# Kernel optimization log

Hardware: AMD Instinct MI355X
Metric: run time of the kernel (lower is better)

Reference implementation:

```python
import jax, jax.numpy as jnp
import numpy as np

B, S, H = 4, 8256, 768
NH, HD = 12, 64
W = 128
SHIFT = W // 2  # 64; first SHIFT tokens form their own block after the shift
NW = (S - SHIFT) // W  # 64 full windows
ROPE_BASE = 10000.0


def _rope_cos_sin(length, hd):
    inv_freq = 1.0 / (ROPE_BASE ** (jnp.arange(0, hd, 2, dtype=jnp.float32) / hd))
    ang = jnp.arange(length, dtype=jnp.float32)[:, None] * inv_freq[None, :]  # [L, hd/2]
    return jnp.cos(ang), jnp.sin(ang)


def _apply_rope(x, cos, sin):
    # x: [..., L, hd]; cos/sin: [L, hd/2] (broadcast over leading dims)
    x1, x2 = x[..., : HD // 2], x[..., HD // 2 :]
    return jnp.concatenate([x1 * cos - x2 * sin, x2 * cos + x1 * sin], axis=-1)


def _sdpa(q, k, v):
    # q,k,v: [..., L, hd]; full softmax attention within the block
    scores = jnp.einsum('...qd,...kd->...qk', q, k) / jnp.sqrt(jnp.asarray(HD, q.dtype))
    probs = jax.nn.softmax(scores, axis=-1)
    return jnp.einsum('...qk,...kd->...qd', probs, v)


def setup_inputs() -> dict:
    key = jax.random.key(0)
    ks = jax.random.split(key, 8)
    std = 0.02
    return {
        'hidden_states': jax.random.normal(ks[0], (B, S, H), dtype=jnp.float32),
        'attention_mask': jnp.zeros((B, 1, 1, S), dtype=jnp.float32),
        'Wq': jax.random.normal(ks[1], (H, H), dtype=jnp.float32) * std,
        'bq': jnp.zeros((H,), dtype=jnp.float32),
        'Wk': jax.random.normal(ks[2], (H, H), dtype=jnp.float32) * std,
        'bk': jnp.zeros((H,), dtype=jnp.float32),
        'Wv': jax.random.normal(ks[3], (H, H), dtype=jnp.float32) * std,
        'bv': jnp.zeros((H,), dtype=jnp.float32),
    }


def _global_block(h, Wq, bq, Wk, bk, Wv, bv):
    # h: [B, L, H]; full attention with global-position RoPE (BertSelfAttention.forward)
    L = h.shape[1]
    cos, sin = _rope_cos_sin(L, HD)

    def heads(x):  # [B, L, H] -> [B, NH, L, HD]
        return x.reshape(B, L, NH, HD).transpose(0, 2, 1, 3)

    q = _apply_rope(heads(h @ Wq.T + bq), cos, sin)
    k = _apply_rope(heads(h @ Wk.T + bk), cos, sin)
    v = heads(h @ Wv.T + bv)
    ctx = _sdpa(q, k, v)  # [B, NH, L, HD]
    return ctx.transpose(0, 2, 1, 3).reshape(B, L, H)


def _local_blocks(h, Wq, bq, Wk, bk, Wv, bv):
    # h: [B, NW*W, H]; per-window attention with window-local RoPE (_mh_local)
    cos, sin = _rope_cos_sin(W, HD)

    def win_heads(x):  # [B, NW*W, H] -> [B, NW, NH, W, HD]
        return x.reshape(B, NW, W, NH, HD).transpose(0, 1, 3, 2, 4)

    q = _apply_rope(win_heads(h @ Wq.T + bq), cos, sin)
    k = _apply_rope(win_heads(h @ Wk.T + bk), cos, sin)
    v = win_heads(h @ Wv.T + bv)
    ctx = _sdpa(q, k, v)  # [B, NW, NH, W, HD]
    return ctx.transpose(0, 1, 3, 2, 4).reshape(B, NW * W, H)


def reference(hidden_states, attention_mask, Wq, bq, Wk, bk, Wv, bv):
    # Shifted local attention: first SHIFT tokens attend among themselves
    # (small global block), the rest is split into NW full windows of size W.
    head = _global_block(hidden_states[:, :SHIFT, :], Wq, bq, Wk, bk, Wv, bv)
    body = _local_blocks(hidden_states[:, SHIFT:, :], Wq, bq, Wk, bk, Wv, bv)
    return jnp.concatenate([head, body], axis=1)  # [B, S, H]
```

## Files before the change

kernel.cpp:

```cpp
#include <hip/hip_runtime.h>
#include <stdint.h>

constexpr int B  = 4, S = 8256, H = 768, NH = 12, HD = 64;
constexpr int M  = B * S;
constexpr int N3 = 3 * H;
constexpr long XB_OFF   = 0;
constexpr long XB_BYTES = (long)M * H * 2;
constexpr long W_OFF    = XB_OFF + XB_BYTES;
constexpr long W_BYTES  = (long)N3 * H * 2;
constexpr long ROPE_OFF = W_OFF + W_BYTES;
constexpr long ROPE_BYTES = 128 * 32 * 2 * 4;
constexpr long QKV_OFF  = ROPE_OFF + ROPE_BYTES;
constexpr long QKV_BYTES = (long)M * N3 * 2;
constexpr long WS_NEEDED = QKV_OFF + QKV_BYTES;

typedef __attribute__((ext_vector_type(8))) _Float16 h8;
typedef __attribute__((ext_vector_type(8))) unsigned short us8;
typedef __attribute__((ext_vector_type(4))) float f4;

#define MFMA16(a,b,c) __builtin_amdgcn_mfma_f32_16x16x32_f16((a),(b),(c),0,0,0)
#define GLL16(gp, lp) __builtin_amdgcn_global_load_lds( \
    (__attribute__((address_space(1))) void*)(gp),      \
    (__attribute__((address_space(3))) void*)(lp), 16, 0, 0)

static __device__ __forceinline__ unsigned short f2h(float x) {
  _Float16 h = (_Float16)x;
  return __builtin_bit_cast(unsigned short, h);
}
static __device__ __forceinline__ f4 f4z() { f4 z = {0.f,0.f,0.f,0.f}; return z; }

__global__ __launch_bounds__(256) void prep_kernel(
    const float* __restrict__ X,
    const float* __restrict__ Wq, const float* __restrict__ Wk, const float* __restrict__ Wv,
    unsigned short* __restrict__ Xb, unsigned short* __restrict__ Wcat, float* __restrict__ rope)
{
  int bid = blockIdx.x;
  if (bid < 12384) {
    long base = (long)bid * 2048 + threadIdx.x * 8;
    float4 v0 = *(const float4*)(X + base);
    float4 v1 = *(const float4*)(X + base + 4);
    us8 o;
    o[0]=f2h(v0.x); o[1]=f2h(v0.y); o[2]=f2h(v0.z); o[3]=f2h(v0.w);
    o[4]=f2h(v1.x); o[5]=f2h(v1.y); o[6]=f2h(v1.z); o[7]=f2h(v1.w);
    *(us8*)(Xb + base) = o;
  } else if (bid < 13248) {
    int wb  = bid - 12384;
    int mat = wb / 288;
    int base = (wb % 288) * 2048 + threadIdx.x * 8;
    const float* src = (mat == 0) ? Wq : (mat == 1) ? Wk : Wv;
    float4 v0 = *(const float4*)(src + base);
    float4 v1 = *(const float4*)(src + base + 4);
    us8 o;
    o[0]=f2h(v0.x); o[1]=f2h(v0.y); o[2]=f2h(v0.z); o[3]=f2h(v0.w);
    o[4]=f2h(v1.x); o[5]=f2h(v1.y); o[6]=f2h(v1.z); o[7]=f2h(v1.w);
    *(us8*)(Wcat + (long)mat * 589824 + base) = o;
  } else {
    int t = (bid - 13248) * 256 + threadIdx.x;
    int p = t >> 5, i = t & 31;
    double ang = (double)p * pow(10000.0, -(double)i / 32.0);
    rope[2*t]   = (float)cos(ang);
    rope[2*t+1] = (float)sin(ang);
  }
}

__global__ __launch_bounds__(256) void qkv_gemm(
    const unsigned short* __restrict__ Xb, const unsigned short* __restrict__ Wb,
    const float* __restrict__ bqp, const float* __restrict__ bkp, const float* __restrict__ bvp,
    const float* __restrict__ rope, unsigned short* __restrict__ QKV)
{
  __shared__ __align__(16) unsigned char ldsA[128 * 128];
  __shared__ __align__(16) unsigned char ldsB[128 * 128];
  const int tid = threadIdx.x, lane = tid & 63, wid = tid >> 6;
  const int bid = blockIdx.x;
  const int mt = bid % (M / 128);
  const int nt = bid / (M / 128);
  const long m0 = (long)mt * 128;
  const int  n0 = nt * 128;
  const int wm = wid >> 1, wn = wid & 1;

  f4 acc[4][4];
  #pragma unroll
  for (int i = 0; i < 4; ++i)
    #pragma unroll
    for (int j = 0; j < 4; ++j) acc[i][j] = f4z();

  const char* Xc = (const char*)Xb;
  const char* Wc = (const char*)Wb;

  for (int kt = 0; kt < 768 / 64; ++kt) {
    const int k0b = kt * 128;
    #pragma unroll
    for (int i = 0; i < 4; ++i) {
      const int ob = ((i << 2) + wid) * 1024;
      const int o  = ob + lane * 16;
      const int row = o >> 7, cb = o & 127;
      const int csrc = cb ^ ((row & 7) << 4);
      GLL16(Xc + (m0 + row) * 1536 + k0b + csrc, ldsA + ob);
      GLL16(Wc + (long)(n0 + row) * 1536 + k0b + csrc, ldsB + ob);
    }
    asm volatile("s_waitcnt vmcnt(0)" ::: "memory");
    __syncthreads();
    #pragma unroll
    for (int ks = 0; ks < 2; ++ks) {
      h8 a[4], b[4];
      const int kb = ks * 64 + ((lane >> 4) << 4);
      #pragma unroll
      for (int f = 0; f < 4; ++f) {
        const int ra = wm * 64 + f * 16 + (lane & 15);
        a[f] = *(const h8*)(ldsA + ra * 128 + (kb ^ ((ra & 7) << 4)));
        const int rb = wn * 64 + f * 16 + (lane & 15);
        b[f] = *(const h8*)(ldsB + rb * 128 + (kb ^ ((rb & 7) << 4)));
      }
      #pragma unroll
      for (int fm = 0; fm < 4; ++fm)
        #pragma unroll
        for (int fn = 0; fn < 4; ++fn)
          acc[fm][fn] = MFMA16(a[fm], b[fn], acc[fm][fn]);
    }
    __syncthreads();
  }

  const int colb = n0 + wn * 64;
  const int sel = (colb >= 1536) ? 2 : (colb >= 768) ? 1 : 0;
  const float* bias = (sel == 0) ? bqp : (sel == 1) ? bkp : bvp;
  const int hcol = colb % 768;
  float bia[4];
  #pragma unroll
  for (int f = 0; f < 4; ++f) bia[f] = bias[hcol + f * 16 + (lane & 15)];

  #pragma unroll
  for (int fm = 0; fm < 4; ++fm) {
    #pragma unroll
    for (int reg = 0; reg < 4; ++reg) {
      const long m = m0 + wm * 64 + fm * 16 + ((lane >> 4) << 2) + reg;
      const int s = (int)(m % (long)S);
      const int pos = (s < 64) ? s : ((s - 64) & 127);
      unsigned short* orow = QKV + m * N3 + colb;
      if (sel < 2) {
        #pragma unroll
        for (int f = 0; f < 2; ++f) {
          const int d1 = f * 16 + (lane & 15);
          const float c  = rope[(pos * 32 + d1) * 2];
          const float sn = rope[(pos * 32 + d1) * 2 + 1];
          const float x1 = acc[fm][f][reg]     + bia[f];
          const float x2 = acc[fm][f + 2][reg] + bia[f + 2];
          orow[f * 16 + (lane & 15)]       = f2h(x1 * c - x2 * sn);
          orow[(f + 2) * 16 + (lane & 15)] = f2h(x2 * c + x1 * sn);
        }
      } else {
        #pragma unroll
        for (int f = 0; f < 4; ++f)
          orow[f * 16 + (lane & 15)] = f2h(acc[fm][f][reg] + bia[f]);
      }
    }
  }
}

template <int T>
__global__ __launch_bounds__(256) void attn_kernel(
    const unsigned short* __restrict__ QKV, float* __restrict__ out)
{
  constexpr int NF  = T / 16;
  constexpr int NKS = T / 32;
  __shared__ __align__(16) unsigned char sVT[16384];
  __shared__ __align__(16) unsigned char sP[4][8192];

  const int tid = threadIdx.x, lane = tid & 63, w = tid >> 6;
  int bid = blockIdx.x;
  const int h = bid % NH; bid /= NH;
  long row0;
  if (T == 64) row0 = (long)bid * S;
  else { const int ww = bid % 64; const int b = bid / 64; row0 = (long)b * S + 64 + (long)ww * 128; }
  const unsigned short* Qb = QKV + row0 * N3 + h * HD;
  const unsigned short* Kb = Qb + H;
  const unsigned short* Vb = Qb + 2 * H;

  {
    const int p = lane;
    if (2 * p + 1 < T) {
      const unsigned short* v0 = Vb + (long)(2 * p) * N3 + w * 16;
      const unsigned short* v1 = v0 + N3;
      us8 a0 = *(const us8*)(v0);
      us8 a1 = *(const us8*)(v0 + 8);
      us8 c0 = *(const us8*)(v1);
      us8 c1 = *(const us8*)(v1 + 8);
      #pragma unroll
      for (int i = 0; i < 8; ++i) {
        const int d = w * 16 + i, d2 = d + 8;
        *(unsigned*)(sVT + d  * 256 + ((4 * p) ^ ((d  & 15) << 4))) = (unsigned)a0[i] | ((unsigned)c0[i] << 16);
        *(unsigned*)(sVT + d2 * 256 + ((4 * p) ^ ((d2 & 15) << 4))) = (unsigned)a1[i] | ((unsigned)c1[i] << 16);
      }
    }
  }
  __syncthreads();

  if (w * 32 < T) {
    h8 aq[2][2];
    #pragma unroll
    for (int fm = 0; fm < 2; ++fm)
      #pragma unroll
      for (int ks = 0; ks < 2; ++ks) {
        const long r = w * 32 + fm * 16 + (lane & 15);
        aq[fm][ks] = *(const h8*)(Qb + r * N3 + ks * 32 + ((lane >> 4) << 3));
      }

    f4 acc[2][NF];
    #pragma unroll
    for (int i = 0; i < 2; ++i)
      #pragma unroll
      for (int f = 0; f < NF; ++f) acc[i][f] = f4z();

    #pragma unroll
    for (int f = 0; f < NF; ++f) {
      const long rk = f * 16 + (lane & 15);
      const unsigned short* kr = Kb + rk * N3 + ((lane >> 4) << 3);
      h8 b0 = *(const h8*)(kr);
      h8 b1 = *(const h8*)(kr + 32);
      acc[0][f] = MFMA16(aq[0][0], b0, acc[0][f]);
      acc[0][f] = MFMA16(aq[0][1], b1, acc[0][f]);
      acc[1][f] = MFMA16(aq[1][0], b0, acc[1][f]);
      acc[1][f] = MFMA16(aq[1][1], b1, acc[1][f]);
    }

    unsigned char* Pw = sP[w];
    #pragma unroll
    for (int fm = 0; fm < 2; ++fm) {
      #pragma unroll
      for (int reg = 0; reg < 4; ++reg) {
        float mx = -3.0e38f;
        #pragma unroll
        for (int f = 0; f < NF; ++f) mx = fmaxf(mx, acc[fm][f][reg]);
        mx = fmaxf(mx, __shfl_xor(mx, 1));
        mx = fmaxf(mx, __shfl_xor(mx, 2));
        mx = fmaxf(mx, __shfl_xor(mx, 4));
        mx = fmaxf(mx, __shfl_xor(mx, 8));
        float pv[NF], sum = 0.f;
        #pragma unroll
        for (int f = 0; f < NF; ++f) {
          const float p = __expf((acc[fm][f][reg] - mx) * 0.125f);
          pv[f] = p; sum += p;
        }
        sum += __shfl_xor(sum, 1);
        sum += __shfl_xor(sum, 2);
        sum += __shfl_xor(sum, 4);
        sum += __shfl_xor(sum, 8);
        const float inv = 1.0f / sum;
        const int rloc = fm * 16 + ((lane >> 4) << 2) + reg;
        const int swz = (rloc & 7) << 4;
        #pragma unroll
        for (int f = 0; f < NF; ++f) {
          const int cb = (f * 16 + (lane & 15)) * 2;
          *(unsigned short*)(Pw + rloc * 256 + (cb ^ swz)) = f2h(pv[f] * inv);
        }
      }
    }

    f4 acc2[2][4];
    #pragma unroll
    for (int i = 0; i < 2; ++i)
      #pragma unroll
      for (int j = 0; j < 4; ++j) acc2[i][j] = f4z();

    #pragma unroll
    for (int ks = 0; ks < NKS; ++ks) {
      h8 pa[2], vb[4];
      const int kb = ks * 64 + ((lane >> 4) << 4);
      #pragma unroll
      for (int fm = 0; fm < 2; ++fm) {
        const int rp = fm * 16 + (lane & 15);
        pa[fm] = *(const h8*)(Pw + rp * 256 + (kb ^ ((rp & 7) << 4)));
      }
      #pragma unroll
      for (int df = 0; df < 4; ++df) {
        const int d = df * 16 + (lane & 15);
        vb[df] = *(const h8*)(sVT + d * 256 + (kb ^ ((d & 15) << 4)));
      }
      #pragma unroll
      for (int fm = 0; fm < 2; ++fm)
        #pragma unroll
        for (int df = 0; df < 4; ++df)
          acc2[fm][df] = MFMA16(pa[fm], vb[df], acc2[fm][df]);
    }

    float* ob = out + (row0 + w * 32) * H + h * HD;
    #pragma unroll
    for (int fm = 0; fm < 2; ++fm)
      #pragma unroll
      for (int df = 0; df < 4; ++df)
        #pragma unroll
        for (int reg = 0; reg < 4; ++reg) {
          const long r = fm * 16 + ((lane >> 4) << 2) + reg;
          const int c = df * 16 + (lane & 15);
          ob[r * H + c] = acc2[fm][df][reg];
        }
  }
}

extern "C" void kernel_launch(void* const* d_in, const int* in_sizes, int n_in,
                              void* d_out, int out_size, void* d_ws, size_t ws_size,
                              hipStream_t stream) {
  const float* X  = (const float*)d_in[0];
  const float* Wq = (const float*)d_in[2];
  const float* bq = (const float*)d_in[3];
  const float* Wk = (const float*)d_in[4];
  const float* bk = (const float*)d_in[5];
  const float* Wv = (const float*)d_in[6];
  const float* bv = (const float*)d_in[7];
  float* out = (float*)d_out;

  if ((long)ws_size < WS_NEEDED) return;

  char* ws = (char*)d_ws;
  unsigned short* Xb   = (unsigned short*)(ws + XB_OFF);
  unsigned short* Wcat = (unsigned short*)(ws + W_OFF);
  float*          rope = (float*)(ws + ROPE_OFF);
  unsigned short* QKV  = (unsigned short*)(ws + QKV_OFF);

  prep_kernel<<<13264, 256, 0, stream>>>(X, Wq, Wk, Wv, Xb, Wcat, rope);
  qkv_gemm<<<(M / 128) * (N3 / 128), 256, 0, stream>>>(Xb, Wcat, bq, bk, bv, rope, QKV);
  attn_kernel<64><<<B * NH, 256, 0, stream>>>(QKV, out);
  attn_kernel<128><<<B * 64 * NH, 256, 0, stream>>>(QKV, out);
}
```

Baseline: 468.6 us.

## Double-buffer QKV GEMM LDS tiles and remap workgroups per XCD

The QKV projection GEMM now double-buffers its LDS tiles. The next K-slice is issued via global_load_lds while the current slice feeds the MFMAs, synchronised with partial vmcnt waits and raw barriers. Workgroup IDs are also remapped so that each XCD gets a contiguous range of tiles in n-fastest order, which improves L2 reuse of the shared X rows across the 18 N-tiles. LDS use doubles to 64KB per block, which may reduce occupancy.

Result: faster. 418.0 us (-10.8%).

```diff
diff --git a/kernel.cpp b/kernel.cpp
--- a/kernel.cpp
+++ b/kernel.cpp
@@ -4,6 +4,8 @@
 constexpr int B  = 4, S = 8256, H = 768, NH = 12, HD = 64;
 constexpr int M  = B * S;
 constexpr int N3 = 3 * H;
+constexpr int NWG_GEMM = (M / 128) * (N3 / 128);
+constexpr int XQ8 = NWG_GEMM / 8, XR8 = NWG_GEMM % 8;
 constexpr long XB_OFF   = 0;
 constexpr long XB_BYTES = (long)M * H * 2;
 constexpr long W_OFF    = XB_OFF + XB_BYTES;
@@ -68,12 +70,15 @@
     const float* __restrict__ bqp, const float* __restrict__ bkp, const float* __restrict__ bvp,
     const float* __restrict__ rope, unsigned short* __restrict__ QKV)
 {
-  __shared__ __align__(16) unsigned char ldsA[128 * 128];
-  __shared__ __align__(16) unsigned char ldsB[128 * 128];
+  __shared__ __align__(16) unsigned char ldsA[2][16384];
+  __shared__ __align__(16) unsigned char ldsB[2][16384];
   const int tid = threadIdx.x, lane = tid & 63, wid = tid >> 6;
-  const int bid = blockIdx.x;
-  const int mt = bid % (M / 128);
-  const int nt = bid / (M / 128);
+
+  const int bid0 = blockIdx.x;
+  const int xcd = bid0 & 7, idx = bid0 >> 3;
+  const int wgid = (xcd < XR8 ? xcd * (XQ8 + 1) : XR8 * (XQ8 + 1) + (xcd - XR8) * XQ8) + idx;
+  const int mt = wgid / 18;
+  const int nt = wgid % 18;
   const long m0 = (long)mt * 128;
   const int  n0 = nt * 128;
   const int wm = wid >> 1, wn = wid & 1;
@@ -87,38 +92,66 @@
   const char* Xc = (const char*)Xb;
   const char* Wc = (const char*)Wb;
 
-  for (int kt = 0; kt < 768 / 64; ++kt) {
-    const int k0b = kt * 128;
-    #pragma unroll
-    for (int i = 0; i < 4; ++i) {
-      const int ob = ((i << 2) + wid) * 1024;
-      const int o  = ob + lane * 16;
-      const int row = o >> 7, cb = o & 127;
-      const int csrc = cb ^ ((row & 7) << 4);
-      GLL16(Xc + (m0 + row) * 1536 + k0b + csrc, ldsA + ob);
-      GLL16(Wc + (long)(n0 + row) * 1536 + k0b + csrc, ldsB + ob);
-    }
-    asm volatile("s_waitcnt vmcnt(0)" ::: "memory");
-    __syncthreads();
-    #pragma unroll
-    for (int ks = 0; ks < 2; ++ks) {
-      h8 a[4], b[4];
-      const int kb = ks * 64 + ((lane >> 4) << 4);
-      #pragma unroll
-      for (int f = 0; f < 4; ++f) {
-        const int ra = wm * 64 + f * 16 + (lane & 15);
-        a[f] = *(const h8*)(ldsA + ra * 128 + (kb ^ ((ra & 7) << 4)));
-        const int rb = wn * 64 + f * 16 + (lane & 15);
-        b[f] = *(const h8*)(ldsB + rb * 128 + (kb ^ ((rb & 7) << 4)));
-      }
-      #pragma unroll
-      for (int fm = 0; fm < 4; ++fm)
-        #pragma unroll
-        for (int fn = 0; fn < 4; ++fn)
-          acc[fm][fn] = MFMA16(a[fm], b[fn], acc[fm][fn]);
-    }
-    __syncthreads();
-  }
+#define STAGE(Abuf, Bbuf, kt) do {                                          \
+    const int k0b_ = (kt) * 128;                                            \
+    _Pragma("unroll")                                                       \
+    for (int i_ = 0; i_ < 4; ++i_) {                                        \
+      const int ob_ = ((i_ << 2) + wid) * 1024;      \
+      const int o_  = ob_ + lane * 16;                \
+      const int row_ = o_ >> 7, cb_ = o_ & 127;                             \
+      const int csrc_ = cb_ ^ ((row_ & 7) << 4);      \
+      GLL16(Xc + (m0 + row_) * 1536 + k0b_ + csrc_, (Abuf) + ob_);          \
+      GLL16(Wc + (long)(n0 + row_) * 1536 + k0b_ + csrc_, (Bbuf) + ob_);    \
+    }                                                                       \
+  } while (0)
+
+#define COMPUTE(Abuf, Bbuf) do {                                            \
+    _Pragma("unroll")                                                       \
+    for (int ks_ = 0; ks_ < 2; ++ks_) {                                     \
+      h8 a_[4], b_[4];                                                      \
+      const int kb_ = ks_ * 64 + ((lane >> 4) << 4);                        \
+      _Pragma("unroll")                                                     \
+      for (int f_ = 0; f_ < 4; ++f_) {                                      \
+        const int ra_ = wm * 64 + f_ * 16 + (lane & 15);                    \
+        a_[f_] = *(const h8*)((Abuf) + ra_ * 128 + (kb_ ^ ((ra_ & 7) << 4)));\
+        const int rb_ = wn * 64 + f_ * 16 + (lane & 15);                    \
+        b_[f_] = *(const h8*)((Bbuf) + rb_ * 128 + (kb_ ^ ((rb_ & 7) << 4)));\
+      }                                                                     \
+      _Pragma("unroll")                                                     \
+      for (int fm_ = 0; fm_ < 4; ++fm_)                                     \
+        _Pragma("unroll")                                                   \
+        for (int fn_ = 0; fn_ < 4; ++fn_)                                   \
+          acc[fm_][fn_] = MFMA16(a_[fm_], b_[fn_], acc[fm_][fn_]);          \
+    }                                                                       \
+  } while (0)
+
+  unsigned char* A0 = ldsA[0];  unsigned char* A1 = ldsA[1];
+  unsigned char* B0 = ldsB[0];  unsigned char* B1 = ldsB[1];
+
+  STAGE(A0, B0, 0);
+  #pragma unroll
+  for (int kt = 0; kt < 12; kt += 2) {
+    STAGE(A1, B1, kt + 1);
+    asm volatile("s_waitcnt vmcnt(8)" ::: "memory");
+    __builtin_amdgcn_s_barrier();
+    asm volatile("" ::: "memory");
+    COMPUTE(A0, B0);
+    asm volatile("" ::: "memory");
+    __builtin_amdgcn_s_barrier();
+    if (kt + 2 < 12) {
+      STAGE(A0, B0, kt + 2);
+      asm volatile("s_waitcnt vmcnt(8)" ::: "memory");
+    } else {
+      asm volatile("s_waitcnt vmcnt(0)" ::: "memory");
+    }
+    __builtin_amdgcn_s_barrier();
+    asm volatile("" ::: "memory");
+    COMPUTE(A1, B1);
+    asm volatile("" ::: "memory");
+    __builtin_amdgcn_s_barrier();
+  }
+#undef STAGE
+#undef COMPUTE
 
   const int colb = n0 + wn * 64;
   const int sel = (colb >= 1536) ? 2 : (colb >= 768) ? 1 : 0;
@@ -317,7 +350,7 @@
   unsigned short* QKV  = (unsigned short*)(ws + QKV_OFF);
 
   prep_kernel<<<13264, 256, 0, stream>>>(X, Wq, Wk, Wv, Xb, Wcat, rope);
-  qkv_gemm<<<(M / 128) * (N3 / 128), 256, 0, stream>>>(Xb, Wcat, bq, bk, bv, rope, QKV);
+  qkv_gemm<<<NWG_GEMM, 256, 0, stream>>>(Xb, Wcat, bq, bk, bv, rope, QKV);
   attn_kernel<64><<<B * NH, 256, 0, stream>>>(QKV, out);
   attn_kernel<128><<<B * 64 * NH, 256, 0, stream>>>(QKV, out);
 }
```
